# Kernel tuning notes

Hardware: AMD Instinct MI355X
Metric: run time of the kernel (lower is better)

The kernel has to match this reference:

```python
import jax, jax.numpy as jnp
import numpy as np

N_NODES = 50000
N_EDGES = 800000
D_IN = 128
D_OUT = 128


def setup_inputs() -> dict:
    key = jax.random.key(0)
    k1, k2, k3, k4, k5 = jax.random.split(key, 5)
    gain = float(np.sqrt(2.0))  # calculate_gain('relu')
    # xavier_uniform bound: gain * sqrt(6/(fan_in+fan_out))
    bound = gain * float(np.sqrt(6.0 / (D_IN + D_OUT)))
    feat = jax.random.normal(k1, (N_NODES, D_IN), dtype=jnp.float32)
    weight = jax.random.uniform(k2, (D_IN, D_OUT), minval=-bound, maxval=bound, dtype=jnp.float32)
    loop_weight = jax.random.uniform(k3, (D_IN, D_OUT), minval=-bound, maxval=bound, dtype=jnp.float32)
    h_bias = jnp.zeros((D_OUT,), dtype=jnp.float32)
    src = jax.random.randint(k4, (N_EDGES,), 0, N_NODES, dtype=jnp.int32)
    dst = jax.random.randint(k5, (N_EDGES,), 0, N_NODES, dtype=jnp.int32)
    return {"feat": feat, "weight": weight, "h_bias": h_bias,
            "loop_weight": loop_weight, "src": src, "dst": dst}


def reference(feat, weight, h_bias, loop_weight, src, dst):
    # message: m_e = feat[src_e] @ W ; aggregate: h_v = sum_{e: dst_e=v} m_e
    # (equivalently transform-then-gather, which avoids the [E, D] matmul)
    transformed = feat @ weight                    # [N, D_out]
    msgs = transformed[src]                        # [E, D_out] gather
    h = jax.ops.segment_sum(msgs, dst, num_segments=feat.shape[0])  # [N, D_out]
    h = h + h_bias                                 # bias
    h = h + feat @ loop_weight                     # self-loop
    # activation=None, dropout=0 -> identity
    return h
```

## Files before the change

### kernel.cpp

```cpp
#include <hip/hip_runtime.h>

#define D 128
#define CAP 64
#define FCHUNK 2048
#define TPAD 68

typedef __attribute__((ext_vector_type(8))) short bf16x8;
typedef __attribute__((ext_vector_type(4))) float f32x4;

__device__ inline unsigned short f2bf_rne(float x) {
    unsigned u = __float_as_uint(x);
    return (unsigned short)((u + 0x7FFFu + ((u >> 16) & 1u)) >> 16);
}
__device__ inline float bf_lo(unsigned u) { return __uint_as_float(u << 16); }
__device__ inline float bf_hi(unsigned u) { return __uint_as_float(u & 0xFFFF0000u); }

__global__ __launch_bounds__(256) void prep_kernel(
    const float* __restrict__ W, const float* __restrict__ LW,
    unsigned short* __restrict__ Bt, int* __restrict__ cursor, int ncur)
{
    int tid = blockIdx.x * 256 + threadIdx.x;
    if (tid < 2 * D * D) {
        int n = tid >> 7;
        int k = tid & 127;
        float v = (n < D) ? W[(size_t)k * D + n] : LW[(size_t)k * D + (n - D)];
        Bt[(size_t)n * D + k] = f2bf_rne(v);
    }
    int j = tid - 2 * D * D;
    if (j >= 0 && j < ncur) cursor[j] = 0;
}

__global__ __launch_bounds__(256, 8) void fill_mfma_kernel(
    const int* __restrict__ src, const int* __restrict__ dst,
    int* __restrict__ cursor, unsigned short* __restrict__ ebuf,
    int E, int cstride, int nmfma,
    const float* __restrict__ feat, const unsigned short* __restrict__ Bt,
    unsigned short* __restrict__ T2, int N)
{
    __shared__ unsigned short tile[4 * 16 * TPAD];
    const int b = blockIdx.x;

    if (b >= nmfma) {
        const int fidx = b - nmfma;
        const int cls  = b & 7;
        const int base = (fidx >> 3) * FCHUNK + threadIdx.x;
#pragma unroll
        for (int ii = 0; ii < FCHUNK / 256; ++ii) {
            const int e  = base + ii * 256;
            const bool ok = (e < E);
            const int d = ok ? dst[e] : -1;
            const int s = ok ? src[e] : 0;
            if (ok && (d & 7) == cls) {
                const int pos = atomicAdd(&cursor[cls * cstride + (d >> 3)], 1);
                if (pos < CAP) ebuf[(size_t)d * CAP + pos] = (unsigned short)s;
            }
        }
        return;
    }

    const int wave = threadIdx.x >> 6;
    const int lane = threadIdx.x & 63;
    const int wrow0 = b * 64 + wave * 16;
    const int m  = lane & 15;
    const int kg = lane >> 4;
    unsigned short* wtile = tile + wave * 16 * TPAD;

    int arow_idx = wrow0 + m;
    if (arow_idx >= N) arow_idx = N - 1;
    const float* arow = feat + (size_t)arow_idx * D;

    bf16x8 a[4];
#pragma unroll
    for (int ks = 0; ks < 4; ++ks) {
        const float4 f0 = *(const float4*)(arow + ks * 32 + kg * 8);
        const float4 f1 = *(const float4*)(arow + ks * 32 + kg * 8 + 4);
        bf16x8 v;
        v[0] = (short)f2bf_rne(f0.x); v[1] = (short)f2bf_rne(f0.y);
        v[2] = (short)f2bf_rne(f0.z); v[3] = (short)f2bf_rne(f0.w);
        v[4] = (short)f2bf_rne(f1.x); v[5] = (short)f2bf_rne(f1.y);
        v[6] = (short)f2bf_rne(f1.z); v[7] = (short)f2bf_rne(f1.w);
        a[ks] = v;
    }

#pragma unroll
    for (int p = 0; p < 4; ++p) {
        f32x4 acc[4];
#pragma unroll
        for (int tt = 0; tt < 4; ++tt) acc[tt] = (f32x4){0.f, 0.f, 0.f, 0.f};

#pragma unroll
        for (int tt = 0; tt < 4; ++tt) {
            const unsigned short* brow = Bt + (size_t)((p * 4 + tt) * 16 + m) * D;
            bf16x8 b0 = *(const bf16x8*)(brow + 0 * 32 + kg * 8);
            bf16x8 b1 = *(const bf16x8*)(brow + 1 * 32 + kg * 8);
            bf16x8 b2 = *(const bf16x8*)(brow + 2 * 32 + kg * 8);
            bf16x8 b3 = *(const bf16x8*)(brow + 3 * 32 + kg * 8);
            acc[tt] = __builtin_amdgcn_mfma_f32_16x16x32_bf16(a[0], b0, acc[tt], 0, 0, 0);
            acc[tt] = __builtin_amdgcn_mfma_f32_16x16x32_bf16(a[1], b1, acc[tt], 0, 0, 0);
            acc[tt] = __builtin_amdgcn_mfma_f32_16x16x32_bf16(a[2], b2, acc[tt], 0, 0, 0);
            acc[tt] = __builtin_amdgcn_mfma_f32_16x16x32_bf16(a[3], b3, acc[tt], 0, 0, 0);
        }

#pragma unroll
        for (int tt = 0; tt < 4; ++tt)
#pragma unroll
            for (int r = 0; r < 4; ++r)
                wtile[(kg * 4 + r) * TPAD + tt * 16 + m] = f2bf_rne(acc[tt][r]);

#pragma unroll
        for (int i = 0; i < 4; ++i) {
            const int f   = i * 64 + lane;
            const int row = f >> 4;
            const int seg = f & 15;
            if (wrow0 + row < N)
                *(uint2*)(T2 + (size_t)(wrow0 + row) * 256 + p * 64 + seg * 4) =
                    *(const uint2*)(wtile + row * TPAD + seg * 4);
        }
    }
}

__global__ __launch_bounds__(256) void gather_kernel(
    const unsigned short* __restrict__ ebuf, const int* __restrict__ cursor,
    const unsigned short* __restrict__ T2, const float* __restrict__ bias,
    float* __restrict__ out, int N, int cstride)
{
    const int cls  = blockIdx.x & 7;
    const int w    = threadIdx.x >> 6;
    const int node = (((int)(blockIdx.x >> 3) * 4 + w) * 8) + cls;
    const int lane = threadIdx.x & 63;
    if (node >= N) return;

    const int h = lane >> 5;
    const int q = lane & 31;

    int deg = cursor[cls * cstride + (node >> 3)];
    if (deg > CAP) deg = CAP;

    const unsigned* region = (const unsigned*)(ebuf + (size_t)node * CAP);
    const unsigned short* Tq = T2 + q * 4;

    float a0 = 0.f, a1 = 0.f, a2 = 0.f, a3 = 0.f;

    for (int j = 0; j < deg; j += 16) {
        uint2 u[8];
#pragma unroll
        for (int k = 0; k < 8; ++k) {
            const unsigned w32 = region[(j >> 1) + k];
            unsigned s = h ? (w32 >> 16) : (w32 & 0xFFFFu);
            if (j + 2 * k + h >= deg) s = 0;
            u[k] = *(const uint2*)(Tq + (size_t)s * 256);
        }
#pragma unroll
        for (int k = 0; k < 8; ++k) {
            const bool live = (j + 2 * k + h) < deg;
            a0 += live ? bf_lo(u[k].x) : 0.f;
            a1 += live ? bf_hi(u[k].x) : 0.f;
            a2 += live ? bf_lo(u[k].y) : 0.f;
            a3 += live ? bf_hi(u[k].y) : 0.f;
        }
    }

    a0 += __shfl_xor(a0, 32, 64);
    a1 += __shfl_xor(a1, 32, 64);
    a2 += __shfl_xor(a2, 32, 64);
    a3 += __shfl_xor(a3, 32, 64);

    if (h == 0) {
        const uint2 sv = *(const uint2*)(T2 + (size_t)node * 256 + 128 + q * 4);
        const float4 b = *(const float4*)(bias + q * 4);
        f32x4 o;
        o.x = b.x + bf_lo(sv.x) + a0;
        o.y = b.y + bf_hi(sv.x) + a1;
        o.z = b.z + bf_lo(sv.y) + a2;
        o.w = b.w + bf_hi(sv.y) + a3;
        __builtin_nontemporal_store(o, (f32x4*)(out + (size_t)node * D + q * 4));
    }
}

extern "C" void kernel_launch(void* const* d_in, const int* in_sizes, int n_in,
                              void* d_out, int out_size, void* d_ws, size_t ws_size,
                              hipStream_t stream) {
    const float* feat = (const float*)d_in[0];
    const float* W    = (const float*)d_in[1];
    const float* bias = (const float*)d_in[2];
    const float* LW   = (const float*)d_in[3];
    const int*   src  = (const int*)d_in[4];
    const int*   dst  = (const int*)d_in[5];
    float* out = (float*)d_out;

    const int N = in_sizes[0] / D;
    const int E = in_sizes[4];
    const int cstride = (N + 7) >> 3;
    const int ncur = 8 * cstride;

    unsigned short* T2   = (unsigned short*)d_ws;
    unsigned short* Bt   = T2 + (size_t)N * 256;
    unsigned short* ebuf = Bt + 2 * D * D;
    int* cursor = (int*)(ebuf + (size_t)N * CAP);

    {
        const int work = 2 * D * D + ncur;
        prep_kernel<<<dim3((work + 255) / 256), 256, 0, stream>>>(W, LW, Bt, cursor, ncur);
    }

    {
        const int nchunks = (E + FCHUNK - 1) / FCHUNK;
        const int nfill   = nchunks * 8;
        const int nmfma   = (N + 63) / 64;
        fill_mfma_kernel<<<dim3(nmfma + nfill), 256, 0, stream>>>(
            src, dst, cursor, ebuf, E, cstride, nmfma, feat, Bt, T2, N);
    }

    {
        const int bpc = (cstride + 3) / 4;
        gather_kernel<<<dim3(8 * bpc), 256, 0, stream>>>(
            ebuf, cursor, T2, bias, out, N, cstride);
    }
}
```

Baseline: 166.0 us.

## Restructure gather to 16B loads, four edges per wave, prefetched edge list

The gather kernel now has each lane load 16 bytes (8 bf16) per neighbor row, with four edge lanes-groups per wave instead of two. It preloads the first 32 neighbor indices and issues up to eight wide row loads up front before a tail loop, and hoists the self-loop row and bias loads ahead of the accumulation. The aim is more memory-level parallelism and fewer latency-bound loop iterations in the gather. The fill chunk size is also halved to spawn more fill blocks. In exchange it uses more registers and an extra shuffle stage for the reduction.

```diff
diff --git a/kernel.cpp b/kernel.cpp
--- a/kernel.cpp
+++ b/kernel.cpp
@@ -2,7 +2,7 @@
 
 #define D 128
 #define CAP 64
-#define FCHUNK 2048
+#define FCHUNK 1024
 #define TPAD 68
 
 typedef __attribute__((ext_vector_type(8))) short bf16x8;
@@ -130,50 +130,76 @@
     const int lane = threadIdx.x & 63;
     if (node >= N) return;
 
-    const int h = lane >> 5;
-    const int q = lane & 31;
-
+    const int r = lane >> 4;
+    const int t = lane & 15;
+
+    const unsigned* region = (const unsigned*)(ebuf + (size_t)node * CAP);
+    const unsigned short* Tt = T2 + t * 8;
+
+    unsigned rw[16];
+#pragma unroll
+    for (int k = 0; k < 16; ++k) rw[k] = region[k];
     int deg = cursor[cls * cstride + (node >> 3)];
+    const uint4 sv = *(const uint4*)(T2 + (size_t)node * 256 + 128 + t * 8);
+    const float4 b0 = *(const float4*)(bias + t * 8);
+    const float4 b1 = *(const float4*)(bias + t * 8 + 4);
     if (deg > CAP) deg = CAP;
 
-    const unsigned* region = (const unsigned*)(ebuf + (size_t)node * CAP);
-    const unsigned short* Tq = T2 + q * 4;
-
     float a0 = 0.f, a1 = 0.f, a2 = 0.f, a3 = 0.f;
-
-    for (int j = 0; j < deg; j += 16) {
-        uint2 u[8];
-#pragma unroll
-        for (int k = 0; k < 8; ++k) {
-            const unsigned w32 = region[(j >> 1) + k];
-            unsigned s = h ? (w32 >> 16) : (w32 & 0xFFFFu);
-            if (j + 2 * k + h >= deg) s = 0;
-            u[k] = *(const uint2*)(Tq + (size_t)s * 256);
-        }
-#pragma unroll
-        for (int k = 0; k < 8; ++k) {
-            const bool live = (j + 2 * k + h) < deg;
-            a0 += live ? bf_lo(u[k].x) : 0.f;
-            a1 += live ? bf_hi(u[k].x) : 0.f;
-            a2 += live ? bf_lo(u[k].y) : 0.f;
-            a3 += live ? bf_hi(u[k].y) : 0.f;
-        }
-    }
-
-    a0 += __shfl_xor(a0, 32, 64);
-    a1 += __shfl_xor(a1, 32, 64);
-    a2 += __shfl_xor(a2, 32, 64);
-    a3 += __shfl_xor(a3, 32, 64);
-
-    if (h == 0) {
-        const uint2 sv = *(const uint2*)(T2 + (size_t)node * 256 + 128 + q * 4);
-        const float4 b = *(const float4*)(bias + q * 4);
-        f32x4 o;
-        o.x = b.x + bf_lo(sv.x) + a0;
-        o.y = b.y + bf_hi(sv.x) + a1;
-        o.z = b.z + bf_lo(sv.y) + a2;
-        o.w = b.w + bf_hi(sv.y) + a3;
-        __builtin_nontemporal_store(o, (f32x4*)(out + (size_t)node * D + q * 4));
+    float a4 = 0.f, a5 = 0.f, a6 = 0.f, a7 = 0.f;
+
+    uint4 u[8];
+#pragma unroll
+    for (int k = 0; k < 8; ++k) {
+        const unsigned w32 = rw[2 * k + (r >> 1)];
+        unsigned s = (r & 1) ? (w32 >> 16) : (w32 & 0xFFFFu);
+        if (4 * k + r >= deg) s = 0;
+        u[k] = *(const uint4*)(Tt + (size_t)s * 256);
+    }
+#pragma unroll
+    for (int k = 0; k < 8; ++k) {
+        const bool live = (4 * k + r) < deg;
+        a0 += live ? bf_lo(u[k].x) : 0.f;
+        a1 += live ? bf_hi(u[k].x) : 0.f;
+        a2 += live ? bf_lo(u[k].y) : 0.f;
+        a3 += live ? bf_hi(u[k].y) : 0.f;
+        a4 += live ? bf_lo(u[k].z) : 0.f;
+        a5 += live ? bf_hi(u[k].z) : 0.f;
+        a6 += live ? bf_lo(u[k].w) : 0.f;
+        a7 += live ? bf_hi(u[k].w) : 0.f;
+    }
+
+    for (int j = 32 + r; j < deg; j += 4) {
+        const unsigned w32 = region[j >> 1];
+        const unsigned s = (j & 1) ? (w32 >> 16) : (w32 & 0xFFFFu);
+        const uint4 uu = *(const uint4*)(Tt + (size_t)s * 256);
+        a0 += bf_lo(uu.x); a1 += bf_hi(uu.x);
+        a2 += bf_lo(uu.y); a3 += bf_hi(uu.y);
+        a4 += bf_lo(uu.z); a5 += bf_hi(uu.z);
+        a6 += bf_lo(uu.w); a7 += bf_hi(uu.w);
+    }
+
+    a0 += __shfl_xor(a0, 16, 64); a0 += __shfl_xor(a0, 32, 64);
+    a1 += __shfl_xor(a1, 16, 64); a1 += __shfl_xor(a1, 32, 64);
+    a2 += __shfl_xor(a2, 16, 64); a2 += __shfl_xor(a2, 32, 64);
+    a3 += __shfl_xor(a3, 16, 64); a3 += __shfl_xor(a3, 32, 64);
+    a4 += __shfl_xor(a4, 16, 64); a4 += __shfl_xor(a4, 32, 64);
+    a5 += __shfl_xor(a5, 16, 64); a5 += __shfl_xor(a5, 32, 64);
+    a6 += __shfl_xor(a6, 16, 64); a6 += __shfl_xor(a6, 32, 64);
+    a7 += __shfl_xor(a7, 16, 64); a7 += __shfl_xor(a7, 32, 64);
+
+    if (r == 0) {
+        f32x4 o0, o1;
+        o0.x = b0.x + bf_lo(sv.x) + a0;
+        o0.y = b0.y + bf_hi(sv.x) + a1;
+        o0.z = b0.z + bf_lo(sv.y) + a2;
+        o0.w = b0.w + bf_hi(sv.y) + a3;
+        o1.x = b1.x + bf_lo(sv.z) + a4;
+        o1.y = b1.y + bf_hi(sv.z) + a5;
+        o1.z = b1.z + bf_lo(sv.w) + a6;
+        o1.w = b1.w + bf_hi(sv.w) + a7;
+        __builtin_nontemporal_store(o0, (f32x4*)(out + (size_t)node * D + t * 8));
+        __builtin_nontemporal_store(o1, (f32x4*)(out + (size_t)node * D + t * 8 + 4));
     }
 }
 
```

New measurement: 179.9 us. 1.08x slower.
